# Optimization experiments

Measured on AMD Instinct MI355X. Metric: run time of the kernel, lower is better.

Reference implementation:

```python
import jax, jax.numpy as jnp
import numpy as np

N = 50000      # nodes
E = 800000     # edges
D_IN = 128
H1, H2 = 256, 128
G = 64         # graphs in batch
NC = 2         # classes
EPS = 1e-5     # batchnorm eps


def setup_inputs() -> dict:
    key = jax.random.key(0)
    ks = jax.random.split(key, 16)
    rn = lambda k, shp: jax.random.normal(k, shp, jnp.float32) * 0.05
    inp = {}
    inp["x"] = jax.random.normal(ks[0], (N, D_IN), jnp.float32)
    inp["edge_index"] = jax.random.randint(ks[1], (2, E), 0, N)
    inp["batch"] = jnp.sort(jax.random.randint(ks[2], (N,), 0, G))
    # SAGE layer 0 (128 -> 256): lin_l (bias) for aggregated, lin_r (no bias) for self
    inp["Wl0"] = rn(ks[3], (D_IN, H1)); inp["bl0"] = jnp.zeros((H1,), jnp.float32)
    inp["Wr0"] = rn(ks[4], (D_IN, H1))
    inp["g0"] = jnp.ones((H1,), jnp.float32); inp["be0"] = jnp.zeros((H1,), jnp.float32)
    # SAGE layer 1 (256 -> 128)
    inp["Wl1"] = rn(ks[5], (H1, H2)); inp["bl1"] = jnp.zeros((H2,), jnp.float32)
    inp["Wr1"] = rn(ks[6], (H1, H2))
    inp["g1"] = jnp.ones((H2,), jnp.float32); inp["be1"] = jnp.zeros((H2,), jnp.float32)
    # residual projections (dims differ at both layers)
    inp["Wp0"] = rn(ks[7], (D_IN, H1)); inp["bp0"] = jnp.zeros((H1,), jnp.float32)
    inp["Wp1"] = rn(ks[8], (H1, H2)); inp["bp1"] = jnp.zeros((H2,), jnp.float32)
    # classifier: Linear(128,256)+BN, Linear(256,128)+BN, Linear(128,2)
    inp["Wc0"] = rn(ks[9], (H2, 256)); inp["bc0"] = jnp.zeros((256,), jnp.float32)
    inp["gc0"] = jnp.ones((256,), jnp.float32); inp["bec0"] = jnp.zeros((256,), jnp.float32)
    inp["Wc1"] = rn(ks[10], (256, 128)); inp["bc1"] = jnp.zeros((128,), jnp.float32)
    inp["gc1"] = jnp.ones((128,), jnp.float32); inp["bec1"] = jnp.zeros((128,), jnp.float32)
    inp["Wc2"] = rn(ks[11], (128, NC)); inp["bc2"] = jnp.zeros((NC,), jnp.float32)
    return inp


def _bn(x, g, b):
    mu = x.mean(0)
    var = x.var(0)
    return g * (x - mu) / jnp.sqrt(var + EPS) + b


def _sage_layer(x, src, dst, Wl, bl, Wr, g, be, n):
    # mean aggregation of neighbor messages: gather x[src], scatter-add to dst
    agg = jax.ops.segment_sum(x[src], dst, num_segments=n)
    cnt = jax.ops.segment_sum(jnp.ones((src.shape[0],), x.dtype), dst, num_segments=n)
    mean = agg / jnp.maximum(cnt, 1.0)[:, None]
    out = mean @ Wl + bl + x @ Wr
    # SAGEConv normalize=True -> L2 normalize rows (F.normalize eps=1e-12)
    out = out / jnp.maximum(jnp.linalg.norm(out, axis=1, keepdims=True), 1e-12)
    return jax.nn.relu(_bn(out, g, be))  # dropout is identity (eval)


def reference(x, edge_index, batch, Wl0, bl0, Wr0, g0, be0, Wl1, bl1, Wr1, g1, be1,
              Wp0, bp0, Wp1, bp1, Wc0, bc0, gc0, bec0, Wc1, bc1, gc1, bec1, Wc2, bc2):
    src, dst = edge_index[0], edge_index[1]
    # layer 0 + residual
    h = _sage_layer(x, src, dst, Wl0, bl0, Wr0, g0, be0, N)
    res = x @ Wp0 + bp0
    h = h + res
    res = h
    # layer 1 + residual
    h = _sage_layer(h, src, dst, Wl1, bl1, Wr1, g1, be1, N)
    res = res @ Wp1 + bp1
    h = h + res
    # global mean pool per graph
    s = jax.ops.segment_sum(h, batch, num_segments=G)
    c = jax.ops.segment_sum(jnp.ones((N,), h.dtype), batch, num_segments=G)
    emb = s / jnp.maximum(c, 1.0)[:, None]
    # classifier MLP
    z = jax.nn.relu(_bn(emb @ Wc0 + bc0, gc0, bec0))
    z = jax.nn.relu(_bn(z @ Wc1 + bc1, gc1, bec1))
    logits = z @ Wc2 + bc2
    return (logits, emb)
```

## Files before the change

kernel.cpp:

```cpp
#include <hip/hip_runtime.h>
#include <hip/hip_bf16.h>
#include <math.h>

#define N_NODES 50000
#define N_EDGES 800000
#define D_IN    128
#define H1_     256
#define H2_     128
#define NG      64
#define NC_     2
#define BN_EPS  1e-5f
#define PAD_    64

typedef __attribute__((ext_vector_type(8))) short bf16x8;
typedef __attribute__((ext_vector_type(4))) float f32x4;

__device__ __forceinline__ float bf2f(unsigned short u) {
    unsigned int v = ((unsigned int)u) << 16;
    return __uint_as_float(v);
}
__device__ __forceinline__ unsigned short f2bf(float f) {
    __hip_bfloat16 h = __float2bfloat16(f);
    return *reinterpret_cast<unsigned short*>(&h);
}

__global__ void degree_kernel(const int* __restrict__ ei, int* __restrict__ deg)
{
    int e = blockIdx.x * 256 + threadIdx.x;
    if (e < N_EDGES) atomicAdd(&deg[ei[N_EDGES + e]], 1);
}

__global__ void fill_kernel(const int* __restrict__ ei, int* __restrict__ cursor,
                            int* __restrict__ ell)
{
    int e = blockIdx.x * 256 + threadIdx.x;
    if (e < N_EDGES) {
        int d = ei[N_EDGES + e];
        int off = atomicAdd(&cursor[d], 1);
        if (off < PAD_) ell[d * PAD_ + off] = ei[e];
    }
}

__global__ void conv_bf16_kernel(const float* __restrict__ in,
                                 unsigned short* __restrict__ out, int n4)
{
    int i = blockIdx.x * 256 + threadIdx.x;
    if (i < n4) {
        float4 v = ((const float4*)in)[i];
        ushort4 o;
        o.x = f2bf(v.x); o.y = f2bf(v.y); o.z = f2bf(v.z); o.w = f2bf(v.w);
        ((ushort4*)out)[i] = o;
    }
}

template<int K1, int K2, int HOUT>
__global__ void wswz_kernel(const float* __restrict__ Wl, const float* __restrict__ Wr,
                            const float* __restrict__ Wp,
                            unsigned short* __restrict__ wt, unsigned short* __restrict__ wrp)
{
    constexpr int NKT_T = (K1 + K2) / 32;
    constexpr int NKT_R = K2 / 32;
    constexpr int NNT = HOUT / 16;
    const int total_t = NNT * NKT_T * 64;
    const int total_r = NNT * NKT_R * 64;
    int idx = blockIdx.x * 256 + threadIdx.x;
    if (idx < total_t) {
        int lane = idx & 63, f = idx >> 6;
        int kt = f % NKT_T, nt = f / NKT_T;
        int col = nt * 16 + (lane & 15);
        int k0 = kt * 32 + (lane >> 4) * 8;
        ushort4 lo, hi;
        unsigned short o[8];
        #pragma unroll
        for (int j = 0; j < 8; ++j) {
            int k = k0 + j;
            float v = (k < K1) ? Wl[(size_t)k * HOUT + col]
                               : Wr[(size_t)(k - K1) * HOUT + col];
            o[j] = f2bf(v);
        }
        lo.x = o[0]; lo.y = o[1]; lo.z = o[2]; lo.w = o[3];
        hi.x = o[4]; hi.y = o[5]; hi.z = o[6]; hi.w = o[7];
        ((ushort4*)wt)[idx * 2]     = lo;
        ((ushort4*)wt)[idx * 2 + 1] = hi;
    } else if (idx < total_t + total_r) {
        int i2 = idx - total_t;
        int lane = i2 & 63, f = i2 >> 6;
        int kt = f % NKT_R, nt = f / NKT_R;
        int col = nt * 16 + (lane & 15);
        int k0 = kt * 32 + (lane >> 4) * 8;
        ushort4 lo, hi;
        unsigned short o[8];
        #pragma unroll
        for (int j = 0; j < 8; ++j)
            o[j] = f2bf(Wp[(size_t)(k0 + j) * HOUT + col]);
        lo.x = o[0]; lo.y = o[1]; lo.z = o[2]; lo.w = o[3];
        hi.x = o[4]; hi.y = o[5]; hi.z = o[6]; hi.w = o[7];
        ((ushort4*)wrp)[i2 * 2]     = lo;
        ((ushort4*)wrp)[i2 * 2 + 1] = hi;
    }
}

template<int D>
__global__ __launch_bounds__(256) void gather_mean_bf16_kernel(
    const unsigned short* __restrict__ xb, const int* __restrict__ deg,
    const int* __restrict__ ell, unsigned short* __restrict__ mean)
{
    constexpr int GT = D / 4;
    constexpr int NGRP = 256 / GT;
    int grp = threadIdx.x / GT;
    int t   = threadIdx.x % GT;
    int n = blockIdx.x * NGRP + grp;
    if (n >= N_NODES) return;
    int dn = deg[n];
    int cnt = min(dn, PAD_);
    const int* lst = ell + n * PAD_;
    const ushort4* xv = (const ushort4*)xb;
    float a0 = 0.f, a1 = 0.f, a2 = 0.f, a3 = 0.f;
    int e = 0;
    for (; e + 1 < cnt; e += 2) {
        int s0 = lst[e], s1 = lst[e + 1];
        ushort4 v0 = xv[(size_t)s0 * GT + t];
        ushort4 v1 = xv[(size_t)s1 * GT + t];
        a0 += bf2f(v0.x) + bf2f(v1.x);
        a1 += bf2f(v0.y) + bf2f(v1.y);
        a2 += bf2f(v0.z) + bf2f(v1.z);
        a3 += bf2f(v0.w) + bf2f(v1.w);
    }
    if (e < cnt) {
        int s0 = lst[e];
        ushort4 v0 = xv[(size_t)s0 * GT + t];
        a0 += bf2f(v0.x); a1 += bf2f(v0.y); a2 += bf2f(v0.z); a3 += bf2f(v0.w);
    }
    float inv = 1.0f / fmaxf((float)dn, 1.0f);
    ushort4 o;
    o.x = f2bf(a0 * inv); o.y = f2bf(a1 * inv);
    o.z = f2bf(a2 * inv); o.w = f2bf(a3 * inv);
    ((ushort4*)mean)[(size_t)n * GT + t] = o;
}

template<int K1, int K2, int HOUT, bool R_BF16>
__global__ __launch_bounds__(256) void gemm_mfma_kernel(
    const unsigned short* __restrict__ meanb,
    const unsigned short* __restrict__ selfb,
    const unsigned short* __restrict__ wt,
    const unsigned short* __restrict__ wrp,
    const float* __restrict__ bl, const float* __restrict__ bp,
    float* __restrict__ tout,
    void* __restrict__ rout,
    float* __restrict__ colsum, float* __restrict__ colsumsq)
{
    constexpr int NKT_T = (K1 + K2) / 32;
    constexpr int NKT_R = K2 / 32;
    constexpr int NKT_M = K1 / 32;
    constexpr int NNT   = HOUT / 16;
    __shared__ float sred_s[4][HOUT];
    __shared__ float sred_q[4][HOUT];

    int tid = threadIdx.x;
    int w = tid >> 6, lane = tid & 63;
    int lm = lane & 15, kq = lane >> 4;
    int arow = blockIdx.x * 64 + w * 16 + lm;
    int lrow = (arow < N_NODES) ? arow : (N_NODES - 1);

    bf16x8 af[NKT_T];
    {
        const unsigned short* mrow = meanb + (size_t)lrow * K1 + kq * 8;
        const unsigned short* srow = selfb + (size_t)lrow * K2 + kq * 8;
        #pragma unroll
        for (int kt = 0; kt < NKT_M; ++kt)
            af[kt] = *(const bf16x8*)(mrow + kt * 32);
        #pragma unroll
        for (int kt = 0; kt < NKT_R; ++kt)
            af[NKT_M + kt] = *(const bf16x8*)(srow + kt * 32);
    }

    int orow0 = blockIdx.x * 64 + w * 16 + kq * 4;
    f32x4 tv[NNT];
    float ssq[4] = {0.f, 0.f, 0.f, 0.f};

    #pragma unroll
    for (int nt = 0; nt < NNT; ++nt) {
        f32x4 acc = {0.f, 0.f, 0.f, 0.f};
        #pragma unroll
        for (int kt = 0; kt < NKT_T; ++kt) {
            bf16x8 bw = *(const bf16x8*)(wt + ((size_t)(nt * NKT_T + kt) * 64 + lane) * 8);
            acc = __builtin_amdgcn_mfma_f32_16x16x32_bf16(af[kt], bw, acc, 0, 0, 0);
        }
        float blj = bl[nt * 16 + lm];
        #pragma unroll
        for (int r = 0; r < 4; ++r) {
            acc[r] += blj;
            ssq[r] += acc[r] * acc[r];
        }
        tv[nt] = acc;

        f32x4 racc = {0.f, 0.f, 0.f, 0.f};
        #pragma unroll
        for (int kt = 0; kt < NKT_R; ++kt) {
            bf16x8 bw = *(const bf16x8*)(wrp + ((size_t)(nt * NKT_R + kt) * 64 + lane) * 8);
            racc = __builtin_amdgcn_mfma_f32_16x16x32_bf16(af[NKT_M + kt], bw, racc, 0, 0, 0);
        }
        float bpj = bp[nt * 16 + lm];
        #pragma unroll
        for (int r = 0; r < 4; ++r) {
            int orow = orow0 + r;
            if (orow < N_NODES) {
                float v = racc[r] + bpj;
                if (R_BF16)
                    ((unsigned short*)rout)[(size_t)orow * HOUT + nt * 16 + lm] = f2bf(v);
                else
                    ((float*)rout)[(size_t)orow * HOUT + nt * 16 + lm] = v;
            }
        }
    }

    #pragma unroll
    for (int off = 1; off <= 8; off <<= 1)
        #pragma unroll
        for (int r = 0; r < 4; ++r)
            ssq[r] += __shfl_xor(ssq[r], off);
    float inv[4];
    #pragma unroll
    for (int r = 0; r < 4; ++r)
        inv[r] = 1.0f / fmaxf(sqrtf(ssq[r]), 1e-12f);

    #pragma unroll
    for (int nt = 0; nt < NNT; ++nt) {
        float cs = 0.f, cq = 0.f;
        #pragma unroll
        for (int r = 0; r < 4; ++r) {
            int orow = orow0 + r;
            float v = tv[nt][r] * inv[r];
            if (orow < N_NODES) {
                tout[(size_t)orow * HOUT + nt * 16 + lm] = v;
                cs += v; cq += v * v;
            }
        }
        cs += __shfl_xor(cs, 16); cs += __shfl_xor(cs, 32);
        cq += __shfl_xor(cq, 16); cq += __shfl_xor(cq, 32);
        if (kq == 0) {
            sred_s[w][nt * 16 + lm] = cs;
            sred_q[w][nt * 16 + lm] = cq;
        }
    }
    __syncthreads();
    if (tid < HOUT) {
        float s = sred_s[0][tid] + sred_s[1][tid] + sred_s[2][tid] + sred_s[3][tid];
        float q = sred_q[0][tid] + sred_q[1][tid] + sred_q[2][tid] + sred_q[3][tid];
        atomicAdd(&colsum[tid], s);
        atomicAdd(&colsumsq[tid], q);
    }
}

template<int H>
__global__ void bn_finalize(const float* __restrict__ colsum, const float* __restrict__ colsumsq,
                            const float* __restrict__ g, const float* __restrict__ be,
                            float* __restrict__ scale, float* __restrict__ shift)
{
    int j = threadIdx.x;
    if (j < H) {
        float mu = colsum[j] / (float)N_NODES;
        float var = colsumsq[j] / (float)N_NODES - mu * mu;
        float sc = g[j] * rsqrtf(var + BN_EPS);
        scale[j] = sc;
        shift[j] = be[j] - mu * sc;
    }
}

__global__ void ew0_kernel(const float4* __restrict__ t, const ushort4* __restrict__ rb,
                           const float* __restrict__ scale, const float* __restrict__ shift,
                           ushort4* __restrict__ h0b)
{
    int gid = blockIdx.x * 256 + threadIdx.x;
    if (gid >= N_NODES * H1_ / 4) return;
    int j4 = gid & (H1_ / 4 - 1);
    float4 sc = *(const float4*)(scale + j4 * 4);
    float4 sh = *(const float4*)(shift + j4 * 4);
    float4 tv = t[gid];
    ushort4 rv = rb[gid];
    ushort4 hb;
    hb.x = f2bf(fmaxf(tv.x * sc.x + sh.x, 0.f) + bf2f(rv.x));
    hb.y = f2bf(fmaxf(tv.y * sc.y + sh.y, 0.f) + bf2f(rv.y));
    hb.z = f2bf(fmaxf(tv.z * sc.z + sh.z, 0.f) + bf2f(rv.z));
    hb.w = f2bf(fmaxf(tv.w * sc.w + sh.w, 0.f) + bf2f(rv.w));
    h0b[gid] = hb;
}

__global__ __launch_bounds__(H2_) void ew1_pool_kernel(
    const float* __restrict__ t, const float* __restrict__ r,
    const float* __restrict__ scale, const float* __restrict__ shift,
    const int* __restrict__ batch,
    float* __restrict__ pooled, float* __restrict__ pcnt)
{
    int j = threadIdx.x;
    int n0 = blockIdx.x * 64;
    int nend = min(n0 + 64, N_NODES);
    float acc = 0.f, cacc = 0.f;
    int run = -1;
    float sc = scale[j], sh = shift[j];
    for (int n = n0; n < nend; ++n) {
        int b = batch[n];
        if (b != run) {
            if (run >= 0) {
                atomicAdd(&pooled[run * H2_ + j], acc);
                if (j == 0) atomicAdd(&pcnt[run], cacc);
            }
            run = b; acc = 0.f; cacc = 0.f;
        }
        float v = t[(size_t)n * H2_ + j] * sc + sh;
        v = fmaxf(v, 0.f) + r[(size_t)n * H2_ + j];
        acc += v;
        cacc += 1.f;
    }
    if (run >= 0) {
        atomicAdd(&pooled[run * H2_ + j], acc);
        if (j == 0) atomicAdd(&pcnt[run], cacc);
    }
}

__global__ void pool_fin_kernel(const float* __restrict__ pooled, const float* __restrict__ pcnt,
                                float* __restrict__ emb, float* __restrict__ emb_out)
{
    int gid = blockIdx.x * blockDim.x + threadIdx.x;
    if (gid < NG * H2_) {
        int g = gid >> 7;
        float v = pooled[gid] / fmaxf(pcnt[g], 1.0f);
        emb[gid] = v;
        emb_out[gid] = v;
    }
}

__global__ __launch_bounds__(1024) void classifier_kernel(
    const float* __restrict__ emb,
    const float* __restrict__ Wc0, const float* __restrict__ bc0,
    const float* __restrict__ gc0, const float* __restrict__ bec0,
    const float* __restrict__ Wc1, const float* __restrict__ bc1,
    const float* __restrict__ gc1, const float* __restrict__ bec1,
    const float* __restrict__ Wc2, const float* __restrict__ bc2,
    float* __restrict__ logits)
{
    __shared__ float es[NG][H2_];
    __shared__ float z0s[NG][256];
    __shared__ float red_s[1024];
    __shared__ float red_q[1024];
    __shared__ float scs[256], shs[256];
    int tid = threadIdx.x;
    for (int i = tid; i < NG * H2_; i += 1024) es[i >> 7][i & 127] = emb[i];
    __syncthreads();

    {
        int j = tid & 255, rg = tid >> 8;
        float acc[16];
        float b = bc0[j];
        #pragma unroll
        for (int r = 0; r < 16; ++r) acc[r] = b;
        #pragma unroll 4
        for (int k = 0; k < H2_; ++k) {
            float w = Wc0[k * 256 + j];
            #pragma unroll
            for (int r = 0; r < 16; ++r) acc[r] += es[rg * 16 + r][k] * w;
        }
        float cs = 0.f, cq = 0.f;
        #pragma unroll
        for (int r = 0; r < 16; ++r) { cs += acc[r]; cq += acc[r] * acc[r]; }
        red_s[rg * 256 + j] = cs;
        red_q[rg * 256 + j] = cq;
        __syncthreads();
        if (tid < 256) {
            float s = red_s[tid] + red_s[256 + tid] + red_s[512 + tid] + red_s[768 + tid];
            float q = red_q[tid] + red_q[256 + tid] + red_q[512 + tid] + red_q[768 + tid];
            float mu = s * (1.0f / NG);
            float var = q * (1.0f / NG) - mu * mu;
            float sc = gc0[tid] * rsqrtf(var + BN_EPS);
            scs[tid] = sc;
            shs[tid] = bec0[tid] - mu * sc;
        }
        __syncthreads();
        float sc = scs[j], sh = shs[j];
        #pragma unroll
        for (int r = 0; r < 16; ++r)
            z0s[rg * 16 + r][j] = fmaxf(acc[r] * sc + sh, 0.f);
    }
    __syncthreads();

    {
        int j = tid & 127, rg = tid >> 7;
        float acc[8];
        float b = bc1[j];
        #pragma unroll
        for (int r = 0; r < 8; ++r) acc[r] = b;
        #pragma unroll 4
        for (int k = 0; k < 256; ++k) {
            float w = Wc1[k * H2_ + j];
            #pragma unroll
            for (int r = 0; r < 8; ++r) acc[r] += z0s[rg * 8 + r][k] * w;
        }
        float cs = 0.f, cq = 0.f;
        #pragma unroll
        for (int r = 0; r < 8; ++r) { cs += acc[r]; cq += acc[r] * acc[r]; }
        red_s[rg * 128 + j] = cs;
        red_q[rg * 128 + j] = cq;
        __syncthreads();
        if (tid < 128) {
            float s = 0.f, q = 0.f;
            #pragma unroll
            for (int g = 0; g < 8; ++g) { s += red_s[g * 128 + tid]; q += red_q[g * 128 + tid]; }
            float mu = s * (1.0f / NG);
            float var = q * (1.0f / NG) - mu * mu;
            float sc = gc1[tid] * rsqrtf(var + BN_EPS);
            scs[tid] = sc;
            shs[tid] = bec1[tid] - mu * sc;
        }
        __syncthreads();
        float sc = scs[j], sh = shs[j];
        #pragma unroll
        for (int r = 0; r < 8; ++r)
            es[rg * 8 + r][j] = fmaxf(acc[r] * sc + sh, 0.f);
    }
    __syncthreads();

    if (tid < NG * NC_) {
        int r2 = tid >> 1, c = tid & 1;
        float acc = bc2[c];
        #pragma unroll 4
        for (int k = 0; k < H2_; ++k) acc += es[r2][k] * Wc2[k * NC_ + c];
        logits[r2 * NC_ + c] = acc;
    }
}

extern "C" void kernel_launch(void* const* d_in, const int* in_sizes, int n_in,
                              void* d_out, int out_size, void* d_ws, size_t ws_size,
                              hipStream_t stream)
{
    const float* x    = (const float*)d_in[0];
    const int*   ei   = (const int*)d_in[1];
    const int*   batch= (const int*)d_in[2];
    const float* Wl0  = (const float*)d_in[3];
    const float* bl0  = (const float*)d_in[4];
    const float* Wr0  = (const float*)d_in[5];
    const float* g0   = (const float*)d_in[6];
    const float* be0  = (const float*)d_in[7];
    const float* Wl1  = (const float*)d_in[8];
    const float* bl1  = (const float*)d_in[9];
    const float* Wr1  = (const float*)d_in[10];
    const float* g1   = (const float*)d_in[11];
    const float* be1  = (const float*)d_in[12];
    const float* Wp0  = (const float*)d_in[13];
    const float* bp0  = (const float*)d_in[14];
    const float* Wp1  = (const float*)d_in[15];
    const float* bp1  = (const float*)d_in[16];
    const float* Wc0  = (const float*)d_in[17];
    const float* bc0  = (const float*)d_in[18];
    const float* gc0  = (const float*)d_in[19];
    const float* bec0 = (const float*)d_in[20];
    const float* Wc1  = (const float*)d_in[21];
    const float* bc1  = (const float*)d_in[22];
    const float* gc1  = (const float*)d_in[23];
    const float* bec1 = (const float*)d_in[24];
    const float* Wc2  = (const float*)d_in[25];
    const float* bc2  = (const float*)d_in[26];

    float* ws = (float*)d_ws;
    float* fs = ws;
    float* colsum0   = fs;
    float* colsumsq0 = fs + 256;
    float* colsum1   = fs + 512;
    float* colsumsq1 = fs + 640;
    float* ss0       = fs + 768;
    float* ss1       = fs + 1280;
    float* pooled    = fs + 1536;
    float* pcnt      = fs + 9728;
    float* emb       = fs + 9792;

    unsigned short* wsz0t = (unsigned short*)(ws + 32768);
    unsigned short* wsz0r = (unsigned short*)(ws + 65536);
    unsigned short* wsz1t = (unsigned short*)(ws + 81920);
    unsigned short* wsz1r = (unsigned short*)(ws + 114688);

    int* deg    = (int*)(ws + 131072);
    int* cursor = deg + 50000;
    int* ell    = cursor + 50000;

    unsigned short* h0b    = (unsigned short*)(ws + 3431072);
    unsigned short* xb     = (unsigned short*)(ws + 9831072);
    unsigned short* meanb0 = (unsigned short*)(ws + 13031072);
    unsigned short* meanb1 = xb;
    float* t0  = ws + 16231072;
    float* t1  = t0;
    float* r1  = t0 + 6400000;
    unsigned short* r0b = (unsigned short*)(ws + 29031072);

    float* logits_out = (float*)d_out;
    float* emb_out    = logits_out + NG * NC_;

    hipMemsetAsync(fs, 0, 32768 * sizeof(float), stream);
    hipMemsetAsync(deg, 0, 100000 * sizeof(int), stream);

    degree_kernel<<<(N_EDGES + 255) / 256, 256, 0, stream>>>(ei, deg);
    fill_kernel<<<(N_EDGES + 255) / 256, 256, 0, stream>>>(ei, cursor, ell);
    conv_bf16_kernel<<<(N_NODES * D_IN / 4 + 255) / 256, 256, 0, stream>>>(
        x, xb, N_NODES * D_IN / 4);
    wswz_kernel<D_IN, D_IN, H1_><<<48, 256, 0, stream>>>(Wl0, Wr0, Wp0, wsz0t, wsz0r);
    wswz_kernel<H1_, H1_, H2_><<<48, 256, 0, stream>>>(Wl1, Wr1, Wp1, wsz1t, wsz1r);

    gather_mean_bf16_kernel<D_IN><<<(N_NODES + 7) / 8, 256, 0, stream>>>(
        xb, deg, ell, meanb0);
    gemm_mfma_kernel<D_IN, D_IN, H1_, true><<<(N_NODES + 63) / 64, 256, 0, stream>>>(
        meanb0, xb, wsz0t, wsz0r, bl0, bp0, t0, r0b, colsum0, colsumsq0);
    bn_finalize<H1_><<<1, H1_, 0, stream>>>(colsum0, colsumsq0, g0, be0, ss0, ss0 + 256);
    ew0_kernel<<<(N_NODES * H1_ / 4 + 255) / 256, 256, 0, stream>>>(
        (const float4*)t0, (const ushort4*)r0b, ss0, ss0 + 256, (ushort4*)h0b);

    gather_mean_bf16_kernel<H1_><<<(N_NODES + 3) / 4, 256, 0, stream>>>(
        h0b, deg, ell, meanb1);
    gemm_mfma_kernel<H1_, H1_, H2_, false><<<(N_NODES + 63) / 64, 256, 0, stream>>>(
        meanb1, h0b, wsz1t, wsz1r, bl1, bp1, t1, r1, colsum1, colsumsq1);
    bn_finalize<H2_><<<1, H2_, 0, stream>>>(colsum1, colsumsq1, g1, be1, ss1, ss1 + 128);
    ew1_pool_kernel<<<(N_NODES + 63) / 64, H2_, 0, stream>>>(
        t1, r1, ss1, ss1 + 128, batch, pooled, pcnt);

    pool_fin_kernel<<<32, 256, 0, stream>>>(pooled, pcnt, emb, emb_out);
    classifier_kernel<<<1, 1024, 0, stream>>>(
        emb, Wc0, bc0, gc0, bec0, Wc1, bc1, gc1, bec1, Wc2, bc2, logits_out);
}
```

Baseline: 569.8 us.

## Stage combined swizzled weights in double-buffered LDS for the MFMA GEMM

Merges the main and residual-projection swizzled weight buffers into one interleaved layout per output tile. The GEMM kernel now loads each tile's weights cooperatively into a double-buffered shared-memory area, prefetching the next tile into registers while it computes the current one. Previously every wave read its weight fragments straight from global memory. The aim is to cut redundant global/L2 weight traffic across the four waves of a block. The cost is extra LDS (up to about 24KB for the first layer), a barrier per output tile, and more registers, which may lower occupancy.

```diff
diff --git a/kernel.cpp b/kernel.cpp
--- a/kernel.cpp
+++ b/kernel.cpp
@@ -56,21 +56,21 @@
 template<int K1, int K2, int HOUT>
 __global__ void wswz_kernel(const float* __restrict__ Wl, const float* __restrict__ Wr,
                             const float* __restrict__ Wp,
-                            unsigned short* __restrict__ wt, unsigned short* __restrict__ wrp)
+                            unsigned short* __restrict__ wcomb)
 {
     constexpr int NKT_T = (K1 + K2) / 32;
     constexpr int NKT_R = K2 / 32;
+    constexpr int F = NKT_T + NKT_R;
     constexpr int NNT = HOUT / 16;
-    const int total_t = NNT * NKT_T * 64;
-    const int total_r = NNT * NKT_R * 64;
     int idx = blockIdx.x * 256 + threadIdx.x;
-    if (idx < total_t) {
-        int lane = idx & 63, f = idx >> 6;
-        int kt = f % NKT_T, nt = f / NKT_T;
-        int col = nt * 16 + (lane & 15);
-        int k0 = kt * 32 + (lane >> 4) * 8;
-        ushort4 lo, hi;
-        unsigned short o[8];
+    if (idx >= NNT * F * 64) return;
+    int lane = idx & 63, fi = idx >> 6;
+    int f = fi % F, nt = fi / F;
+    int col = nt * 16 + (lane & 15);
+    int kq8 = (lane >> 4) * 8;
+    unsigned short o[8];
+    if (f < NKT_T) {
+        int k0 = f * 32 + kq8;
         #pragma unroll
         for (int j = 0; j < 8; ++j) {
             int k = k0 + j;
@@ -78,26 +78,17 @@
                                : Wr[(size_t)(k - K1) * HOUT + col];
             o[j] = f2bf(v);
         }
-        lo.x = o[0]; lo.y = o[1]; lo.z = o[2]; lo.w = o[3];
-        hi.x = o[4]; hi.y = o[5]; hi.z = o[6]; hi.w = o[7];
-        ((ushort4*)wt)[idx * 2]     = lo;
-        ((ushort4*)wt)[idx * 2 + 1] = hi;
-    } else if (idx < total_t + total_r) {
-        int i2 = idx - total_t;
-        int lane = i2 & 63, f = i2 >> 6;
-        int kt = f % NKT_R, nt = f / NKT_R;
-        int col = nt * 16 + (lane & 15);
-        int k0 = kt * 32 + (lane >> 4) * 8;
-        ushort4 lo, hi;
-        unsigned short o[8];
+    } else {
+        int k0 = (f - NKT_T) * 32 + kq8;
         #pragma unroll
         for (int j = 0; j < 8; ++j)
             o[j] = f2bf(Wp[(size_t)(k0 + j) * HOUT + col]);
-        lo.x = o[0]; lo.y = o[1]; lo.z = o[2]; lo.w = o[3];
-        hi.x = o[4]; hi.y = o[5]; hi.z = o[6]; hi.w = o[7];
-        ((ushort4*)wrp)[i2 * 2]     = lo;
-        ((ushort4*)wrp)[i2 * 2 + 1] = hi;
-    }
+    }
+    ushort4 lo, hi;
+    lo.x = o[0]; lo.y = o[1]; lo.z = o[2]; lo.w = o[3];
+    hi.x = o[4]; hi.y = o[5]; hi.z = o[6]; hi.w = o[7];
+    ((ushort4*)wcomb)[idx * 2]     = lo;
+    ((ushort4*)wcomb)[idx * 2 + 1] = hi;
 }
 
 template<int D>
@@ -142,8 +133,7 @@
 __global__ __launch_bounds__(256) void gemm_mfma_kernel(
     const unsigned short* __restrict__ meanb,
     const unsigned short* __restrict__ selfb,
-    const unsigned short* __restrict__ wt,
-    const unsigned short* __restrict__ wrp,
+    const unsigned short* __restrict__ wcomb,
     const float* __restrict__ bl, const float* __restrict__ bp,
     float* __restrict__ tout,
     void* __restrict__ rout,
@@ -152,7 +142,11 @@
     constexpr int NKT_T = (K1 + K2) / 32;
     constexpr int NKT_R = K2 / 32;
     constexpr int NKT_M = K1 / 32;
+    constexpr int F     = NKT_T + NKT_R;
     constexpr int NNT   = HOUT / 16;
+    constexpr int CH    = F / 4;
+    constexpr int F64   = F * 64;
+    __shared__ unsigned short wbuf[2][F * 512];
     __shared__ float sred_s[4][HOUT];
     __shared__ float sred_q[4][HOUT];
 
@@ -174,16 +168,35 @@
             af[NKT_M + kt] = *(const bf16x8*)(srow + kt * 32);
     }
 
+    const uint4* wsrc = (const uint4*)wcomb;
+    uint4 st[CH];
+    #pragma unroll
+    for (int i = 0; i < CH; ++i) st[i] = wsrc[i * 256 + tid];
+    {
+        uint4* dst = (uint4*)&wbuf[0][0];
+        #pragma unroll
+        for (int i = 0; i < CH; ++i) dst[i * 256 + tid] = st[i];
+    }
+
     int orow0 = blockIdx.x * 64 + w * 16 + kq * 4;
     f32x4 tv[NNT];
     float ssq[4] = {0.f, 0.f, 0.f, 0.f};
+    int cur = 0;
 
     #pragma unroll
     for (int nt = 0; nt < NNT; ++nt) {
+        if (nt + 1 < NNT) {
+            #pragma unroll
+            for (int i = 0; i < CH; ++i)
+                st[i] = wsrc[(size_t)(nt + 1) * F64 + i * 256 + tid];
+        }
+        __syncthreads();
+
+        const unsigned short* wb = wbuf[cur];
         f32x4 acc = {0.f, 0.f, 0.f, 0.f};
         #pragma unroll
         for (int kt = 0; kt < NKT_T; ++kt) {
-            bf16x8 bw = *(const bf16x8*)(wt + ((size_t)(nt * NKT_T + kt) * 64 + lane) * 8);
+            bf16x8 bw = *(const bf16x8*)(wb + kt * 512 + lane * 8);
             acc = __builtin_amdgcn_mfma_f32_16x16x32_bf16(af[kt], bw, acc, 0, 0, 0);
         }
         float blj = bl[nt * 16 + lm];
@@ -197,7 +210,7 @@
         f32x4 racc = {0.f, 0.f, 0.f, 0.f};
         #pragma unroll
         for (int kt = 0; kt < NKT_R; ++kt) {
-            bf16x8 bw = *(const bf16x8*)(wrp + ((size_t)(nt * NKT_R + kt) * 64 + lane) * 8);
+            bf16x8 bw = *(const bf16x8*)(wb + (NKT_T + kt) * 512 + lane * 8);
             racc = __builtin_amdgcn_mfma_f32_16x16x32_bf16(af[NKT_M + kt], bw, racc, 0, 0, 0);
         }
         float bpj = bp[nt * 16 + lm];
@@ -212,6 +225,13 @@
                     ((float*)rout)[(size_t)orow * HOUT + nt * 16 + lm] = v;
             }
         }
+
+        if (nt + 1 < NNT) {
+            uint4* dst = (uint4*)&wbuf[cur ^ 1][0];
+            #pragma unroll
+            for (int i = 0; i < CH; ++i) dst[i * 256 + tid] = st[i];
+        }
+        cur ^= 1;
     }
 
     #pragma unroll
@@ -472,10 +492,8 @@
     float* pcnt      = fs + 9728;
     float* emb       = fs + 9792;
 
-    unsigned short* wsz0t = (unsigned short*)(ws + 32768);
-    unsigned short* wsz0r = (unsigned short*)(ws + 65536);
-    unsigned short* wsz1t = (unsigned short*)(ws + 81920);
-    unsigned short* wsz1r = (unsigned short*)(ws + 114688);
+    unsigned short* wcomb0 = (unsigned short*)(ws + 32768);
+    unsigned short* wcomb1 = (unsigned short*)(ws + 81920);
 
     int* deg    = (int*)(ws + 131072);
     int* cursor = deg + 50000;
@@ -500,13 +518,13 @@
     fill_kernel<<<(N_EDGES + 255) / 256, 256, 0, stream>>>(ei, cursor, ell);
     conv_bf16_kernel<<<(N_NODES * D_IN / 4 + 255) / 256, 256, 0, stream>>>(
         x, xb, N_NODES * D_IN / 4);
-    wswz_kernel<D_IN, D_IN, H1_><<<48, 256, 0, stream>>>(Wl0, Wr0, Wp0, wsz0t, wsz0r);
-    wswz_kernel<H1_, H1_, H2_><<<48, 256, 0, stream>>>(Wl1, Wr1, Wp1, wsz1t, wsz1r);
+    wswz_kernel<D_IN, D_IN, H1_><<<48, 256, 0, stream>>>(Wl0, Wr0, Wp0, wcomb0);
+    wswz_kernel<H1_, H1_, H2_><<<48, 256, 0, stream>>>(Wl1, Wr1, Wp1, wcomb1);
 
     gather_mean_bf16_kernel<D_IN><<<(N_NODES + 7) / 8, 256, 0, stream>>>(
         xb, deg, ell, meanb0);
     gemm_mfma_kernel<D_IN, D_IN, H1_, true><<<(N_NODES + 63) / 64, 256, 0, stream>>>(
-        meanb0, xb, wsz0t, wsz0r, bl0, bp0, t0, r0b, colsum0, colsumsq0);
+        meanb0, xb, wcomb0, bl0, bp0, t0, r0b, colsum0, colsumsq0);
     bn_finalize<H1_><<<1, H1_, 0, stream>>>(colsum0, colsumsq0, g0, be0, ss0, ss0 + 256);
     ew0_kernel<<<(N_NODES * H1_ / 4 + 255) / 256, 256, 0, stream>>>(
         (const float4*)t0, (const ushort4*)r0b, ss0, ss0 + 256, (ushort4*)h0b);
@@ -514,7 +532,7 @@
     gather_mean_bf16_kernel<H1_><<<(N_NODES + 3) / 4, 256, 0, stream>>>(
         h0b, deg, ell, meanb1);
     gemm_mfma_kernel<H1_, H1_, H2_, false><<<(N_NODES + 63) / 64, 256, 0, stream>>>(
-        meanb1, h0b, wsz1t, wsz1r, bl1, bp1, t1, r1, colsum1, colsumsq1);
+        meanb1, h0b, wcomb1, bl1, bp1, t1, r1, colsum1, colsumsq1);
     bn_finalize<H2_><<<1, H2_, 0, stream>>>(colsum1, colsumsq1, g1, be1, ss1, ss1 + 128);
     ew1_pool_kernel<<<(N_NODES + 63) / 64, H2_, 0, stream>>>(
         t1, r1, ss1, ss1 + 128, batch, pooled, pcnt);
```

Measured after the change: 584.1 us. 1.03x slower.
